# Optimization experiments

Hardware: AMD Instinct MI355X
Metric: run time of the kernel (lower is better)

The kernel has to match this reference:

```python
import jax, jax.numpy as jnp
import numpy as np

B, S, D = 2048, 200, 192  # batch, seq_len, total_dim
H1, H2 = 64, 32
IN = 4 * D


def prelu(x, a):
    return jnp.where(x >= 0, x, a * x)


def setup_inputs() -> dict:
    key = jax.random.key(0)
    ks = jax.random.split(key, 10)
    scale = lambda fan_in: 1.0 / np.sqrt(fan_in)
    return {
        "query": jax.random.normal(ks[0], (B, D), jnp.float32),
        "keys": jax.random.normal(ks[1], (B, S, D), jnp.float32),
        "keys_mask": jax.random.randint(ks[2], (B, S), 0, 2, jnp.int32),
        "W1": jax.random.uniform(ks[3], (IN, H1), jnp.float32, -scale(IN), scale(IN)),
        "b1": jnp.zeros((H1,), jnp.float32),
        "a1": jnp.asarray(0.25, jnp.float32),  # PReLU default slope
        "W2": jax.random.uniform(ks[4], (H1, H2), jnp.float32, -scale(H1), scale(H1)),
        "b2": jnp.zeros((H2,), jnp.float32),
        "a2": jnp.asarray(0.25, jnp.float32),
        "W3": jax.random.uniform(ks[5], (H2, 1), jnp.float32, -scale(H2), scale(H2)),
        "b3": jnp.zeros((1,), jnp.float32),
    }


def reference(query, keys, keys_mask, W1, b1, a1, W2, b2, a2, W3, b3):
    q = query[:, None, :]  # [B,1,D] broadcasts against keys [B,S,D]
    qe = jnp.broadcast_to(q, keys.shape)
    x = jnp.concatenate([keys, qe, keys * qe, keys - qe], axis=-1)  # [B,S,4D]
    h = prelu(jnp.einsum("bsi,ih->bsh", x, W1) + b1, a1)
    h = prelu(jnp.einsum("bsh,hk->bsk", h, W2) + b2, a2)
    scores = (jnp.einsum("bsk,ko->bso", h, W3) + b3)[..., 0]  # [B,S]
    scores = jnp.where(keys_mask.astype(bool), scores, -jnp.inf)
    w = jax.nn.softmax(scores, axis=-1)
    w = jnp.where(jnp.isnan(w), jnp.zeros_like(w), w)
    weighted_sum = jnp.einsum("bs,bsd->bd", w, keys)
    return weighted_sum, w
```

## Files before the change

### kernel.cpp

```cpp
#include <hip/hip_runtime.h>


#define B_N 2048
#define S_N 200
#define D_N 192

typedef __bf16 bf16x8 __attribute__((ext_vector_type(8)));
typedef __bf16 bf16x4 __attribute__((ext_vector_type(4)));
typedef float  f32x4  __attribute__((ext_vector_type(4)));

struct __align__(16) Smem {
  unsigned char kbuf[64*400];
  union {
    unsigned char h1buf[64*144];
    unsigned char w2t[32*144];
  };
  union {
    float qbuf[192];
    float scores[256];
  };
  float cbuf[64];
  union {
    float cpart[4][64];
    float opart[4][192];
  };
  unsigned char maskbuf[256];
  float wm[4], wl[4];
  float w3buf[32];
  float b2buf[32];
  float consts[4];
};

__global__ __launch_bounds__(256, 4) void rich_attn_kernel(
    const float* __restrict__ query, const float* __restrict__ keys,
    const int*   __restrict__ keys_mask, const float* __restrict__ W1,
    const float* __restrict__ b1, const float* __restrict__ a1,
    const float* __restrict__ W2, const float* __restrict__ b2,
    const float* __restrict__ a2, const float* __restrict__ W3,
    const float* __restrict__ b3, float* __restrict__ out)
{
  __shared__ Smem sm;
  const int tid  = threadIdx.x;
  const int b    = blockIdx.x;
  const int wave = tid >> 6;
  const int lane = tid & 63;
  const int quad = (tid >> 4) & 3;
  const int n16  = tid & 15;

  if (tid < 192) sm.qbuf[tid] = query[b*D_N + tid];
  sm.maskbuf[tid] = (tid < 200) ? (unsigned char)(keys_mask[b*S_N + tid] != 0) : 0;
  if (tid < 32)  sm.w3buf[tid] = W3[tid];
  else if (tid < 64) sm.b2buf[tid-32] = b2[tid-32];
  if (tid == 64) { sm.consts[0] = a1[0]; sm.consts[1] = a2[0]; sm.consts[2] = b3[0]; }
  for (int i = tid; i < 64*32; i += 256) {
    int hh = i >> 5, kk = i & 31;
    *((__bf16*)&sm.w2t[kk*144 + hh*2]) = (__bf16)W2[i];
  }
  __syncthreads();

  {
    int hh = tid & 63, pp = tid >> 6;
    float acc = 0.f;
    int d0 = pp*48;
    #pragma unroll 4
    for (int d = d0; d < d0+48; ++d)
      acc += sm.qbuf[d] * (W1[(192+d)*64 + hh] - W1[(576+d)*64 + hh]);
    sm.cpart[pp][hh] = acc;
  }
  bf16x8 fb1[6];
  {
    int h = (wave << 4) | n16;
    #pragma unroll
    for (int t = 0; t < 6; ++t) {
      #pragma unroll
      for (int j = 0; j < 8; ++j) {
        int d = t*32 + quad*8 + j;
        float v = W1[d*64 + h] + W1[(576+d)*64 + h] + sm.qbuf[d]*W1[(384+d)*64 + h];
        fb1[t][j] = (__bf16)v;
      }
    }
  }
  bf16x8 fw2[2][2];
  #pragma unroll
  for (int nt2 = 0; nt2 < 2; ++nt2)
    #pragma unroll
    for (int t = 0; t < 2; ++t)
      fw2[nt2][t] = *(const bf16x8*)&sm.w2t[(nt2*16 + n16)*144 + (t*32 + quad*8)*2];
  const float w3v0 = sm.w3buf[n16],      w3v1 = sm.w3buf[16 + n16];
  const float bbv0 = sm.b2buf[n16],      bbv1 = sm.b2buf[16 + n16];
  const float a1v = sm.consts[0], a2v = sm.consts[1], b3v = sm.consts[2];
  __syncthreads();
  if (tid < 64)
    sm.cbuf[tid] = b1[tid] + sm.cpart[0][tid] + sm.cpart[1][tid]
                 + sm.cpart[2][tid] + sm.cpart[3][tid];

  const float* kb = keys + (size_t)b * (S_N * D_N);
  float m_run = -1e30f, l_run = 0.f;
  f32x4 o = {0.f, 0.f, 0.f, 0.f};

  for (int tile = 0; tile < 4; ++tile) {
    const int s0 = tile * 64;
    #pragma unroll
    for (int i = 0; i < 12; ++i) {
      int f = tid + i*256;
      int row = f / 48, c4 = f % 48;
      int sg = s0 + row;
      float4 v = make_float4(0.f, 0.f, 0.f, 0.f);
      if (sg < 200) v = ((const float4*)kb)[sg*48 + c4];
      bf16x4 bv; bv[0]=(__bf16)v.x; bv[1]=(__bf16)v.y; bv[2]=(__bf16)v.z; bv[3]=(__bf16)v.w;
      *(bf16x4*)&sm.kbuf[row*400 + c4*8] = bv;
    }
    __syncthreads();

    f32x4 acc1[4];
    #pragma unroll
    for (int mt = 0; mt < 4; ++mt) acc1[mt] = (f32x4){0.f,0.f,0.f,0.f};
    #pragma unroll
    for (int mt = 0; mt < 4; ++mt)
      #pragma unroll
      for (int t = 0; t < 6; ++t) {
        bf16x8 fa = *(const bf16x8*)&sm.kbuf[(mt*16 + n16)*400 + (t*32 + quad*8)*2];
        acc1[mt] = __builtin_amdgcn_mfma_f32_16x16x32_bf16(fa, fb1[t], acc1[mt], 0, 0, 0);
      }
    {
      int h = (wave << 4) | n16;
      float cb = sm.cbuf[h];
      #pragma unroll
      for (int mt = 0; mt < 4; ++mt)
        #pragma unroll
        for (int r = 0; r < 4; ++r) {
          int m = mt*16 + quad*4 + r;
          float v = acc1[mt][r] + cb;
          v = (v >= 0.f) ? v : a1v * v;
          *((__bf16*)&sm.h1buf[m*144 + h*2]) = (__bf16)v;
        }
    }
    __syncthreads();

    bf16x8 fa2[2];
    #pragma unroll
    for (int t = 0; t < 2; ++t)
      fa2[t] = *(const bf16x8*)&sm.h1buf[(wave*16 + n16)*144 + (t*32 + quad*8)*2];
    f32x4 acc2[2];
    acc2[0] = (f32x4){0.f,0.f,0.f,0.f};
    acc2[1] = (f32x4){0.f,0.f,0.f,0.f};
    #pragma unroll
    for (int nt2 = 0; nt2 < 2; ++nt2)
      #pragma unroll
      for (int t = 0; t < 2; ++t)
        acc2[nt2] = __builtin_amdgcn_mfma_f32_16x16x32_bf16(fa2[t], fw2[nt2][t], acc2[nt2], 0, 0, 0);

    float sc[4];
    #pragma unroll
    for (int r = 0; r < 4; ++r) {
      float v0 = acc2[0][r] + bbv0; v0 = (v0 >= 0.f) ? v0 : a2v * v0;
      float v1 = acc2[1][r] + bbv1; v1 = (v1 >= 0.f) ? v1 : a2v * v1;
      sc[r] = v0 * w3v0 + v1 * w3v1;
    }
    #pragma unroll
    for (int off = 1; off < 16; off <<= 1)
      #pragma unroll
      for (int r = 0; r < 4; ++r) sc[r] += __shfl_xor(sc[r], off);

    float p[4];
    float mloc = -1e30f;
    #pragma unroll
    for (int r = 0; r < 4; ++r) {
      int sg = s0 + wave*16 + quad*4 + r;
      sc[r] += b3v;
      bool valid = (sg < 200) && (sm.maskbuf[sg] != 0);
      sc[r] = valid ? sc[r] : -1e30f;
      mloc = fmaxf(mloc, sc[r]);
    }
    if (n16 == 0) {
      #pragma unroll
      for (int r = 0; r < 4; ++r) sm.scores[s0 + wave*16 + quad*4 + r] = sc[r];
    }
    mloc = fmaxf(mloc, __shfl_xor(mloc, 16));
    mloc = fmaxf(mloc, __shfl_xor(mloc, 32));
    float m_new = fmaxf(m_run, mloc);
    float fac = __expf(m_run - m_new);
    float psum = 0.f;
    #pragma unroll
    for (int r = 0; r < 4; ++r) {
      p[r] = (sc[r] > -1e29f) ? __expf(sc[r] - m_new) : 0.f;
      psum += p[r];
    }
    psum += __shfl_xor(psum, 16);
    psum += __shfl_xor(psum, 32);
    l_run = l_run * fac + psum;
    m_run = m_new;

    o[0] *= fac; o[1] *= fac; o[2] *= fac; o[3] *= fac;
    #pragma unroll
    for (int s2 = 0; s2 < 16; ++s2) {
      float pvs = __shfl(p[s2 & 3], (s2 >> 2) * 16);
      if (lane < 48) {
        bf16x4 kv = *(const bf16x4*)&sm.kbuf[(wave*16 + s2)*400 + lane*8];
        o[0] += pvs * (float)kv[0];
        o[1] += pvs * (float)kv[1];
        o[2] += pvs * (float)kv[2];
        o[3] += pvs * (float)kv[3];
      }
    }
    __syncthreads();
  }

  if (lane == 0) { sm.wm[wave] = m_run; sm.wl[wave] = l_run; }
  if (lane < 48) *(f32x4*)&sm.opart[wave][lane*4] = o;
  __syncthreads();
  float mg = fmaxf(fmaxf(sm.wm[0], sm.wm[1]), fmaxf(sm.wm[2], sm.wm[3]));
  float e0 = __expf(sm.wm[0] - mg), e1 = __expf(sm.wm[1] - mg);
  float e2 = __expf(sm.wm[2] - mg), e3 = __expf(sm.wm[3] - mg);
  float lg = sm.wl[0]*e0 + sm.wl[1]*e1 + sm.wl[2]*e2 + sm.wl[3]*e3;
  float invl = (lg > 0.f) ? 1.f / lg : 0.f;
  if (tid < 192) {
    float os = sm.opart[0][tid]*e0 + sm.opart[1][tid]*e1
             + sm.opart[2][tid]*e2 + sm.opart[3][tid]*e3;
    out[(size_t)b * D_N + tid] = os * invl;
  }
  if (tid < 200) {
    float wv = (lg > 0.f) ? __expf(sm.scores[tid] - mg) * invl : 0.f;
    out[(size_t)B_N * D_N + (size_t)b * S_N + tid] = wv;
  }
}

extern "C" void kernel_launch(void* const* d_in, const int* in_sizes, int n_in,
                              void* d_out, int out_size, void* d_ws, size_t ws_size,
                              hipStream_t stream) {
  const float* query     = (const float*)d_in[0];
  const float* keys      = (const float*)d_in[1];
  const int*   keys_mask = (const int*)  d_in[2];
  const float* W1        = (const float*)d_in[3];
  const float* b1        = (const float*)d_in[4];
  const float* a1        = (const float*)d_in[5];
  const float* W2        = (const float*)d_in[6];
  const float* b2        = (const float*)d_in[7];
  const float* a2        = (const float*)d_in[8];
  const float* W3        = (const float*)d_in[9];
  const float* b3        = (const float*)d_in[10];
  float* out = (float*)d_out;
  rich_attn_kernel<<<dim3(B_N), dim3(256), 0, stream>>>(
      query, keys, keys_mask, W1, b1, a1, W2, b2, a2, W3, b3, out);
}
```

Before: 537.9 us.

## Give each wave its own 64-row slice; load keys directly into MFMA fragments

Each wave now handles a contiguous 64-row slice of the sequence, so the per-tile block-wide __syncthreads go away. Key rows are loaded straight from global memory into registers as bf16 A-fragments, and the fused W1 matrix is staged in shared memory instead of being held in registers. The weighted-sum pass re-reads keys in fp32 from global/L2 rather than from an LDS bf16 copy, which adds memory traffic but drops the shared key staging and changes the precision of the output sum. Launch bounds are lowered from 4 to 3 blocks per CU, and readfirstlane is used on the scalar constants.

```diff
diff --git a/kernel.cpp b/kernel.cpp
--- a/kernel.cpp
+++ b/kernel.cpp
@@ -6,13 +6,16 @@
 #define D_N 192
 
 typedef __bf16 bf16x8 __attribute__((ext_vector_type(8)));
-typedef __bf16 bf16x4 __attribute__((ext_vector_type(4)));
 typedef float  f32x4  __attribute__((ext_vector_type(4)));
 
+__device__ __forceinline__ float rfl(float x) {
+  return __uint_as_float(__builtin_amdgcn_readfirstlane(__float_as_uint(x)));
+}
+
 struct __align__(16) Smem {
-  unsigned char kbuf[64*400];
+  unsigned char mt[64*400];
   union {
-    unsigned char h1buf[64*144];
+    unsigned char h1w[4][16*144];
     unsigned char w2t[32*144];
   };
   union {
@@ -31,7 +34,7 @@
   float consts[4];
 };
 
-__global__ __launch_bounds__(256, 4) void rich_attn_kernel(
+__global__ __launch_bounds__(256, 3) void rich_attn_kernel(
     const float* __restrict__ query, const float* __restrict__ keys,
     const int*   __restrict__ keys_mask, const float* __restrict__ W1,
     const float* __restrict__ b1, const float* __restrict__ a1,
@@ -67,17 +70,19 @@
       acc += sm.qbuf[d] * (W1[(192+d)*64 + hh] - W1[(576+d)*64 + hh]);
     sm.cpart[pp][hh] = acc;
   }
-  bf16x8 fb1[6];
   {
     int h = (wave << 4) | n16;
     #pragma unroll
     for (int t = 0; t < 6; ++t) {
+      bf16x8 fb;
       #pragma unroll
       for (int j = 0; j < 8; ++j) {
         int d = t*32 + quad*8 + j;
         float v = W1[d*64 + h] + W1[(576+d)*64 + h] + sm.qbuf[d]*W1[(384+d)*64 + h];
-        fb1[t][j] = (__bf16)v;
-      }
+        fb[j] = (__bf16)v;
+      }
+      *(bf16x8*)&sm.mt[h*400 + (t*32 + quad*8)*2] = fb;
+      __builtin_amdgcn_sched_barrier(0);
     }
   }
   bf16x8 fw2[2][2];
@@ -88,59 +93,59 @@
       fw2[nt2][t] = *(const bf16x8*)&sm.w2t[(nt2*16 + n16)*144 + (t*32 + quad*8)*2];
   const float w3v0 = sm.w3buf[n16],      w3v1 = sm.w3buf[16 + n16];
   const float bbv0 = sm.b2buf[n16],      bbv1 = sm.b2buf[16 + n16];
-  const float a1v = sm.consts[0], a2v = sm.consts[1], b3v = sm.consts[2];
+  const float a1v = rfl(sm.consts[0]), a2v = rfl(sm.consts[1]), b3v = rfl(sm.consts[2]);
   __syncthreads();
   if (tid < 64)
     sm.cbuf[tid] = b1[tid] + sm.cpart[0][tid] + sm.cpart[1][tid]
                  + sm.cpart[2][tid] + sm.cpart[3][tid];
+  __syncthreads();
 
   const float* kb = keys + (size_t)b * (S_N * D_N);
+  const int s0 = wave * 64;
   float m_run = -1e30f, l_run = 0.f;
   f32x4 o = {0.f, 0.f, 0.f, 0.f};
 
-  for (int tile = 0; tile < 4; ++tile) {
-    const int s0 = tile * 64;
-    #pragma unroll
-    for (int i = 0; i < 12; ++i) {
-      int f = tid + i*256;
-      int row = f / 48, c4 = f % 48;
-      int sg = s0 + row;
-      float4 v = make_float4(0.f, 0.f, 0.f, 0.f);
-      if (sg < 200) v = ((const float4*)kb)[sg*48 + c4];
-      bf16x4 bv; bv[0]=(__bf16)v.x; bv[1]=(__bf16)v.y; bv[2]=(__bf16)v.z; bv[3]=(__bf16)v.w;
-      *(bf16x4*)&sm.kbuf[row*400 + c4*8] = bv;
-    }
-    __syncthreads();
-
-    f32x4 acc1[4];
-    #pragma unroll
-    for (int mt = 0; mt < 4; ++mt) acc1[mt] = (f32x4){0.f,0.f,0.f,0.f};
-    #pragma unroll
-    for (int mt = 0; mt < 4; ++mt)
+  for (int mt = 0; mt < 4; ++mt) {
+    const int r0 = s0 + mt*16;
+
+    bf16x8 fa[6];
+    {
+      int row = r0 + n16;
+      bool rv = row < 200;
+      const float* kr = kb + (size_t)row * D_N + quad*8;
       #pragma unroll
       for (int t = 0; t < 6; ++t) {
-        bf16x8 fa = *(const bf16x8*)&sm.kbuf[(mt*16 + n16)*400 + (t*32 + quad*8)*2];
-        acc1[mt] = __builtin_amdgcn_mfma_f32_16x16x32_bf16(fa, fb1[t], acc1[mt], 0, 0, 0);
-      }
-    {
-      int h = (wave << 4) | n16;
-      float cb = sm.cbuf[h];
-      #pragma unroll
-      for (int mt = 0; mt < 4; ++mt)
-        #pragma unroll
-        for (int r = 0; r < 4; ++r) {
-          int m = mt*16 + quad*4 + r;
-          float v = acc1[mt][r] + cb;
-          v = (v >= 0.f) ? v : a1v * v;
-          *((__bf16*)&sm.h1buf[m*144 + h*2]) = (__bf16)v;
+        float4 u0 = make_float4(0.f,0.f,0.f,0.f), u1 = make_float4(0.f,0.f,0.f,0.f);
+        if (rv) {
+          u0 = *(const float4*)(kr + t*32);
+          u1 = *(const float4*)(kr + t*32 + 4);
         }
-    }
-    __syncthreads();
+        fa[t][0]=(__bf16)u0.x; fa[t][1]=(__bf16)u0.y; fa[t][2]=(__bf16)u0.z; fa[t][3]=(__bf16)u0.w;
+        fa[t][4]=(__bf16)u1.x; fa[t][5]=(__bf16)u1.y; fa[t][6]=(__bf16)u1.z; fa[t][7]=(__bf16)u1.w;
+      }
+    }
+
+    #pragma unroll
+    for (int nt = 0; nt < 4; ++nt) {
+      f32x4 acc = (f32x4){0.f,0.f,0.f,0.f};
+      #pragma unroll
+      for (int t = 0; t < 6; ++t) {
+        bf16x8 fb = *(const bf16x8*)&sm.mt[(nt*16 + n16)*400 + (t*32 + quad*8)*2];
+        acc = __builtin_amdgcn_mfma_f32_16x16x32_bf16(fa[t], fb, acc, 0, 0, 0);
+      }
+      float cbv = sm.cbuf[nt*16 + n16];
+      #pragma unroll
+      for (int r = 0; r < 4; ++r) {
+        float v = acc[r] + cbv;
+        v = (v >= 0.f) ? v : a1v * v;
+        *((__bf16*)&sm.h1w[wave][(quad*4 + r)*144 + (nt*16 + n16)*2]) = (__bf16)v;
+      }
+    }
 
     bf16x8 fa2[2];
     #pragma unroll
     for (int t = 0; t < 2; ++t)
-      fa2[t] = *(const bf16x8*)&sm.h1buf[(wave*16 + n16)*144 + (t*32 + quad*8)*2];
+      fa2[t] = *(const bf16x8*)&sm.h1w[wave][n16*144 + (t*32 + quad*8)*2];
     f32x4 acc2[2];
     acc2[0] = (f32x4){0.f,0.f,0.f,0.f};
     acc2[1] = (f32x4){0.f,0.f,0.f,0.f};
@@ -166,7 +171,7 @@
     float mloc = -1e30f;
     #pragma unroll
     for (int r = 0; r < 4; ++r) {
-      int sg = s0 + wave*16 + quad*4 + r;
+      int sg = r0 + quad*4 + r;
       sc[r] += b3v;
       bool valid = (sg < 200) && (sm.maskbuf[sg] != 0);
       sc[r] = valid ? sc[r] : -1e30f;
@@ -174,7 +179,7 @@
     }
     if (n16 == 0) {
       #pragma unroll
-      for (int r = 0; r < 4; ++r) sm.scores[s0 + wave*16 + quad*4 + r] = sc[r];
+      for (int r = 0; r < 4; ++r) sm.scores[r0 + quad*4 + r] = sc[r];
     }
     mloc = fmaxf(mloc, __shfl_xor(mloc, 16));
     mloc = fmaxf(mloc, __shfl_xor(mloc, 32));
@@ -195,15 +200,15 @@
     #pragma unroll
     for (int s2 = 0; s2 < 16; ++s2) {
       float pvs = __shfl(p[s2 & 3], (s2 >> 2) * 16);
-      if (lane < 48) {
-        bf16x4 kv = *(const bf16x4*)&sm.kbuf[(wave*16 + s2)*400 + lane*8];
-        o[0] += pvs * (float)kv[0];
-        o[1] += pvs * (float)kv[1];
-        o[2] += pvs * (float)kv[2];
-        o[3] += pvs * (float)kv[3];
-      }
-    }
-    __syncthreads();
+      int g = r0 + s2;
+      if (lane < 48 && g < 200) {
+        float4 kv = *(const float4*)(kb + (size_t)g * D_N + lane*4);
+        o[0] += pvs * kv.x;
+        o[1] += pvs * kv.y;
+        o[2] += pvs * kv.z;
+        o[3] += pvs * kv.w;
+      }
+    }
   }
 
   if (lane == 0) { sm.wm[wave] = m_run; sm.wl[wave] = l_run; }
```

New measurement: 505.7 us. 6.0% less time.
